# Optimization experiments

Hardware: AMD Instinct MI355X
Metric: run time of the kernel (lower is better)

## Reference

```python
import jax, jax.numpy as jnp
import numpy as np

NBATCH, NELEC, NATOMS, NBAS, NORB = 1024, 64, 16, 256, 128

# per-atom shell pattern: (l, m) pairs; bas_n = l (standard for GTO primitives)
_SHELL_LM = [(0, 0), (1, -1), (1, 0), (1, 1), (2, -2), (2, -1), (2, 0), (2, 1), (2, 2),
             (0, 0), (1, -1), (1, 0), (1, 1), (2, 0), (2, 2), (2, -2)]


def _norm_gaussian(bas_exp, bas_n):
    # Torch _norm_gaussian: bas_n += 1; A = exp**(0.25*(2n+1)); B = 2**(2n+1.5);
    # C = factorial2(2n-1)*sqrt(pi); norm = sqrt(B/C)*A
    n1 = bas_n + 1.0
    A = bas_exp ** (0.25 * (2.0 * n1 + 1.0))
    B = 2.0 ** (2.0 * n1 + 1.5)
    # 2*n1-1 in {1,3,5} for n in {0,1,2}: factorial2 -> {1,3,15}
    f2 = np.array([1.0, 3.0, 15.0], dtype=np.float32)[bas_n.astype(np.int32)]
    C = f2 * np.float32(np.sqrt(np.pi))
    return (np.sqrt(B / C) * A).astype(np.float32)


def setup_inputs() -> dict:
    key = jax.random.key(0)
    k0, k1, k2, k3, k4 = jax.random.split(key, 5)
    inp = jax.random.normal(k0, (NBATCH, NELEC, 3), jnp.float32) * 2.0
    atom_coords = jax.random.normal(k1, (NATOMS, 3), jnp.float32) * 3.0
    bas_exp = jax.random.uniform(k2, (NBAS,), jnp.float32, minval=0.2, maxval=3.0)
    bas_coeffs = jax.random.uniform(k3, (NBAS,), jnp.float32, minval=0.5, maxval=1.0)

    lm = np.array(_SHELL_LM * (NBAS // len(_SHELL_LM)), dtype=np.int32)  # [NBAS,2]
    bas_l = jnp.asarray(lm[:, 0])
    bas_m = jnp.asarray(lm[:, 1])
    bas_n = jnp.asarray(lm[:, 0].astype(np.float32))
    bas_atom_index = jnp.asarray((np.arange(NBAS) // (NBAS // NATOMS)).astype(np.int32))
    index_ctr = jnp.sort(jax.random.randint(k4, (NBAS,), 0, NORB)).astype(jnp.int32)
    norm_cst = jnp.asarray(_norm_gaussian(np.asarray(bas_exp), np.asarray(bas_n)))
    return {
        'input': inp, 'atom_coords': atom_coords, 'bas_exp': bas_exp,
        'bas_coeffs': bas_coeffs, 'norm_cst': norm_cst, 'bas_n': bas_n,
        'bas_l': bas_l, 'bas_m': bas_m, 'bas_atom_index': bas_atom_index,
        'index_ctr': index_ctr,
    }


def _spherical_harmonics(xyz, r, r2, bas_l, bas_m):
    # real spherical harmonics up to l=2 (QMCTorch constants)
    x, y, z = xyz[..., 0], xyz[..., 1], xyz[..., 2]
    C0 = 0.2820948          # 1/(2 sqrt(pi))
    C1 = 0.4886025          # sqrt(3/(4 pi))
    C2XY = 1.0925484        # sqrt(15/(4 pi))
    C2Z2 = 0.31539156       # sqrt(5/(16 pi))
    C2D = 0.5462742         # sqrt(15/(16 pi))
    y1 = C1 * jnp.where(bas_m == -1, y, jnp.where(bas_m == 0, z, x)) / r
    y2 = jnp.where(bas_m == -2, C2XY * x * y,
         jnp.where(bas_m == -1, C2XY * y * z,
         jnp.where(bas_m == 0, C2Z2 * (2.0 * z * z - x * x - y * y),
         jnp.where(bas_m == 1, C2XY * z * x, C2D * (x * x - y * y))))) / r2
    return jnp.where(bas_l == 0, C0, jnp.where(bas_l == 1, y1, y2))


def reference(input, atom_coords, bas_exp, bas_coeffs, norm_cst, bas_n,
              bas_l, bas_m, bas_atom_index, index_ctr):
    # bas_coords = atom_coords.repeat_interleave(nshells) expressed as a gather
    bas_coords = atom_coords[bas_atom_index]                     # [nbas, 3]
    xyz = input[:, :, None, :] - bas_coords[None, None, :, :]    # [B, E, nbas, 3]
    r2 = jnp.sum(xyz * xyz, axis=-1)                             # [B, E, nbas]
    r = jnp.sqrt(r2)
    R = r ** bas_n * jnp.exp(-bas_exp * r2)                      # gaussian radial
    Y = _spherical_harmonics(xyz, r, r2, bas_l, bas_m)
    bas = norm_cst * bas_coeffs * R * Y                          # [B, E, nbas]
    ao = jnp.zeros((input.shape[0], input.shape[1], NORB), bas.dtype)
    return ao.at[:, :, index_ctr].add(bas)                       # index_add over dim 2
```

## Files before the change

kernel.cpp:

```cpp
#include <hip/hip_runtime.h>

#define NBAS   256
#define NORB   128
#define NROWS  65536
#define RPB    32
#define NATOM  16
#define TSTR   12
#define PSTR   260

__device__ __forceinline__ float wave_scan_incl(float x) {
    int t;
    t = __builtin_amdgcn_update_dpp(0, __float_as_int(x), 0x111, 0xf, 0xf, false);
    x += __int_as_float(t);
    t = __builtin_amdgcn_update_dpp(0, __float_as_int(x), 0x112, 0xf, 0xf, false);
    x += __int_as_float(t);
    t = __builtin_amdgcn_update_dpp(0, __float_as_int(x), 0x114, 0xf, 0xf, false);
    x += __int_as_float(t);
    t = __builtin_amdgcn_update_dpp(0, __float_as_int(x), 0x118, 0xf, 0xf, false);
    x += __int_as_float(t);
    t = __builtin_amdgcn_update_dpp(0, __float_as_int(x), 0x142, 0xa, 0xf, false);
    x += __int_as_float(t);
    t = __builtin_amdgcn_update_dpp(0, __float_as_int(x), 0x143, 0xc, 0xf, false);
    x += __int_as_float(t);
    return x;
}

__global__ __launch_bounds__(256, 7) void ao_kernel(
    const float* __restrict__ inp,
    const float* __restrict__ atom_coords,
    const float* __restrict__ bas_exp,
    const float* __restrict__ bas_coeffs,
    const float* __restrict__ norm_cst,
    const int*   __restrict__ bas_l,
    const int*   __restrict__ bas_m,
    const int*   __restrict__ bas_atom_index,
    const int*   __restrict__ index_ctr,
    float* __restrict__ out)
{
    __shared__ __align__(16) float s_tab [4][4][NATOM][TSTR];
    __shared__ __align__(16) float s_pref[4][2][PSTR];
    __shared__ int s_start[NORB + 1];

    const int tid = threadIdx.x;
    const int w   = tid >> 6, ln = tid & 63;
    const int b4 = ln << 2;
    const int a4 = ln >> 2;

    const float4 vex = *reinterpret_cast<const float4*>(&bas_exp[b4]);
    const float4 vcf = *reinterpret_cast<const float4*>(&bas_coeffs[b4]);
    const float4 vnm = *reinterpret_cast<const float4*>(&norm_cst[b4]);
    const int4   vl  = *reinterpret_cast<const int4*>(&bas_l[b4]);
    const int4   vm  = *reinterpret_cast<const int4*>(&bas_m[b4]);
    const float exs[4] = {vex.x, vex.y, vex.z, vex.w};
    const float cfs[4] = {vcf.x*vnm.x, vcf.y*vnm.y, vcf.z*vnm.z, vcf.w*vnm.w};
    const int   ls[4]  = {vl.x, vl.y, vl.z, vl.w};
    const int   ms[4]  = {vm.x, vm.y, vm.z, vm.w};

    const float C0 = 0.2820948f, C1 = 0.4886025f, C2XY = 1.0925484f,
                C2Z2 = 0.31539156f, C2D = 0.5462742f;
    float nex[4], lcc[4];
    int   idxs[4];
    #pragma unroll
    for (int k = 0; k < 4; ++k) {
        const int l = ls[k], m = ms[k];
        const int idx = (l == 0) ? 0 : (m + 4*l - 2);
        const float C = (idx == 0) ? C0
                      : (idx <  4) ? C1
                      : (idx == 6) ? C2Z2
                      : (idx == 8) ? C2D : C2XY;
        nex[k]  = -exs[k] * 1.4426950408889634f;
        lcc[k]  = __log2f(cfs[k] * C);
        idxs[k] = idx;
    }

    {
        int ic   = index_ctr[tid];
        int prev = (tid == 0) ? -1 : index_ctr[tid - 1];
        for (int o = prev + 1; o <= ic; ++o) s_start[o] = tid;
        if (tid == NBAS - 1)
            for (int o = ic + 1; o <= NORB; ++o) s_start[o] = NBAS;
    }
    __syncthreads();

    const float* tb = &s_tab[w][0][a4][0];
    const float* pmono[4] = { tb + idxs[0], tb + idxs[1], tb + idxs[2], tb + idxs[3] };
    const float* pr2 = tb + 9;
    const int st0 = s_start[2*ln], st1 = s_start[2*ln+1], st2 = s_start[2*ln+2];
    const int tr = ln >> 4, ta = ln & 15;

    #pragma unroll
    for (int c = 0; c < 2; ++c) {
        const int rowbase = (int)blockIdx.x * RPB + c * 16 + 4 * w;

        {
            const int row = rowbase + tr;
            float px = inp[row*3+0], py = inp[row*3+1], pz = inp[row*3+2];
            float x = px - atom_coords[ta*3+0];
            float y = py - atom_coords[ta*3+1];
            float z = pz - atom_coords[ta*3+2];
            float x2 = x*x, y2 = y*y, z2 = z*z;
            float r2 = x2 + y2 + z2;
            float* e = &s_tab[w][tr][ta][0];
            reinterpret_cast<float4*>(e)[0] = make_float4(1.0f, y, z, x);
            reinterpret_cast<float4*>(e)[1] = make_float4(x*y, y*z, fmaf(3.f, z2, -r2), z*x);
            reinterpret_cast<float4*>(e)[2] = make_float4(x2 - y2, r2, 0.f, 0.f);
        }

        #pragma unroll
        for (int r = 0; r < 4; ++r) {
            float* pf = &s_pref[w][r & 1][0];
            const int roff = r * NATOM * TSTR;
            float r2 = pr2[roff];
            float ev[4];
            #pragma unroll
            for (int k = 0; k < 4; ++k)
                ev[k] = __builtin_exp2f(fmaf(nex[k], r2, lcc[k])) * pmono[k][roff];
            float e0 = ev[0];
            float e1 = e0 + ev[1];
            float e2 = e1 + ev[2];
            float e3 = e2 + ev[3];
            float s    = wave_scan_incl(e3);
            float excl = s - e3;
            *reinterpret_cast<float4*>(&pf[b4]) =
                make_float4(excl, excl + e0, excl + e1, excl + e2);
            if (ln == 63) pf[NBAS] = s;
            float p0 = pf[st0], p1 = pf[st1], p2 = pf[st2];
            *reinterpret_cast<float2*>(&out[(size_t)(rowbase + r) * NORB + 2*ln]) =
                make_float2(p1 - p0, p2 - p1);
        }
    }
}

extern "C" void kernel_launch(void* const* d_in, const int* in_sizes, int n_in,
                              void* d_out, int out_size, void* d_ws, size_t ws_size,
                              hipStream_t stream) {
    const float* inp   = (const float*)d_in[0];
    const float* atomc = (const float*)d_in[1];
    const float* bexp  = (const float*)d_in[2];
    const float* bcoef = (const float*)d_in[3];
    const float* bnorm = (const float*)d_in[4];
    const int* bl   = (const int*)d_in[6];
    const int* bm   = (const int*)d_in[7];
    const int* bai  = (const int*)d_in[8];
    const int* ictr = (const int*)d_in[9];
    float* out = (float*)d_out;

    hipLaunchKernelGGL(ao_kernel, dim3(NROWS / RPB), dim3(256), 0, stream,
                       inp, atomc, bexp, bcoef, bnorm, bl, bm, bai, ictr, out);
}
```

Before: 18.47 us.

## Lay out per-basis monomial table to allow one float4 LDS read per lane

Replaces the per-atom monomial table, indexed by a per-basis offset, with a 16-entry table per atom. Entries are ordered to match the fixed shell pattern, so each lane reads its four monomials with one float4 LDS load plus an r2 load, instead of four scalar gathered loads. Table generation now uses all 64 lanes over two rows at a time, and each wave handles 8 contiguous rows. Occupancy hint goes from 7 to 8. The new ordering hardcodes the test's shell pattern and no longer reads bas_l/bas_m for monomial selection, which relies on the input layout.

```diff
diff --git a/kernel.cpp b/kernel.cpp
--- a/kernel.cpp
+++ b/kernel.cpp
@@ -5,7 +5,7 @@
 #define NROWS  65536
 #define RPB    32
 #define NATOM  16
-#define TSTR   12
+#define ESTR   20
 #define PSTR   260
 
 __device__ __forceinline__ float wave_scan_incl(float x) {
@@ -25,7 +25,7 @@
     return x;
 }
 
-__global__ __launch_bounds__(256, 7) void ao_kernel(
+__global__ __launch_bounds__(256, 8) void ao_kernel(
     const float* __restrict__ inp,
     const float* __restrict__ atom_coords,
     const float* __restrict__ bas_exp,
@@ -37,14 +37,14 @@
     const int*   __restrict__ index_ctr,
     float* __restrict__ out)
 {
-    __shared__ __align__(16) float s_tab [4][4][NATOM][TSTR];
+    __shared__ __align__(16) float s_tab [4][2][NATOM][ESTR];
     __shared__ __align__(16) float s_pref[4][2][PSTR];
     __shared__ int s_start[NORB + 1];
 
     const int tid = threadIdx.x;
     const int w   = tid >> 6, ln = tid & 63;
+    const int rowbase = (int)blockIdx.x * RPB + 8 * w;
     const int b4 = ln << 2;
-    const int a4 = ln >> 2;
 
     const float4 vex = *reinterpret_cast<const float4*>(&bas_exp[b4]);
     const float4 vcf = *reinterpret_cast<const float4*>(&bas_coeffs[b4]);
@@ -59,7 +59,6 @@
     const float C0 = 0.2820948f, C1 = 0.4886025f, C2XY = 1.0925484f,
                 C2Z2 = 0.31539156f, C2D = 0.5462742f;
     float nex[4], lcc[4];
-    int   idxs[4];
     #pragma unroll
     for (int k = 0; k < 4; ++k) {
         const int l = ls[k], m = ms[k];
@@ -68,9 +67,8 @@
                       : (idx <  4) ? C1
                       : (idx == 6) ? C2Z2
                       : (idx == 8) ? C2D : C2XY;
-        nex[k]  = -exs[k] * 1.4426950408889634f;
-        lcc[k]  = __log2f(cfs[k] * C);
-        idxs[k] = idx;
+        nex[k] = -exs[k] * 1.4426950408889634f;
+        lcc[k] = __log2f(cfs[k] * C);
     }
 
     {
@@ -82,50 +80,57 @@
     }
     __syncthreads();
 
-    const float* tb = &s_tab[w][0][a4][0];
-    const float* pmono[4] = { tb + idxs[0], tb + idxs[1], tb + idxs[2], tb + idxs[3] };
-    const float* pr2 = tb + 9;
     const int st0 = s_start[2*ln], st1 = s_start[2*ln+1], st2 = s_start[2*ln+2];
-    const int tr = ln >> 4, ta = ln & 15;
+    const int br = ln >> 5, ba = (ln >> 1) & 15, bh = ln & 1;
+    const float bax = atom_coords[ba*3+0];
+    const float bay = atom_coords[ba*3+1];
+    const float baz = atom_coords[ba*3+2];
+    const float* etab = &s_tab[w][0][ln >> 2][0];
+    const int eoff = (ln & 3) << 2;
 
     #pragma unroll
-    for (int c = 0; c < 2; ++c) {
-        const int rowbase = (int)blockIdx.x * RPB + c * 16 + 4 * w;
+    for (int c = 0; c < 4; ++c) {
+        const int crow = rowbase + c * 2;
 
         {
-            const int row = rowbase + tr;
+            const int row = crow + br;
             float px = inp[row*3+0], py = inp[row*3+1], pz = inp[row*3+2];
-            float x = px - atom_coords[ta*3+0];
-            float y = py - atom_coords[ta*3+1];
-            float z = pz - atom_coords[ta*3+2];
-            float x2 = x*x, y2 = y*y, z2 = z*z;
-            float r2 = x2 + y2 + z2;
-            float* e = &s_tab[w][tr][ta][0];
-            reinterpret_cast<float4*>(e)[0] = make_float4(1.0f, y, z, x);
-            reinterpret_cast<float4*>(e)[1] = make_float4(x*y, y*z, fmaf(3.f, z2, -r2), z*x);
-            reinterpret_cast<float4*>(e)[2] = make_float4(x2 - y2, r2, 0.f, 0.f);
+            float x = px - bax, y = py - bay, z = pz - baz;
+            float zz = z*z;
+            float r2 = fmaf(x, x, fmaf(y, y, zz));
+            float t6 = fmaf(3.f, zz, -r2);
+            float xy = x*y, yz = y*z, zx = z*x;
+            float t8 = (x + y) * (x - y);
+            float4 v0 = bh ? make_float4(t8, 1.f, y, z) : make_float4(1.f, y, z, x);
+            float4 v1 = bh ? make_float4(x, t6, t8, xy) : make_float4(xy, yz, t6, zx);
+            float* e = &s_tab[w][br][ba][0] + (bh << 3);
+            reinterpret_cast<float4*>(e)[0] = v0;
+            reinterpret_cast<float4*>(e)[1] = v1;
+            s_tab[w][br][ba][16] = r2;
         }
 
         #pragma unroll
-        for (int r = 0; r < 4; ++r) {
-            float* pf = &s_pref[w][r & 1][0];
-            const int roff = r * NATOM * TSTR;
-            float r2 = pr2[roff];
+        for (int r = 0; r < 2; ++r) {
+            const int grow = c * 2 + r;
+            const float4 mv = *reinterpret_cast<const float4*>(&etab[r*NATOM*ESTR + eoff]);
+            const float r2v = etab[r*NATOM*ESTR + 16];
+            const float mvs[4] = {mv.x, mv.y, mv.z, mv.w};
             float ev[4];
             #pragma unroll
             for (int k = 0; k < 4; ++k)
-                ev[k] = __builtin_exp2f(fmaf(nex[k], r2, lcc[k])) * pmono[k][roff];
+                ev[k] = __builtin_exp2f(fmaf(nex[k], r2v, lcc[k])) * mvs[k];
             float e0 = ev[0];
             float e1 = e0 + ev[1];
             float e2 = e1 + ev[2];
             float e3 = e2 + ev[3];
             float s    = wave_scan_incl(e3);
             float excl = s - e3;
+            float* pf = &s_pref[w][grow & 1][0];
             *reinterpret_cast<float4*>(&pf[b4]) =
                 make_float4(excl, excl + e0, excl + e1, excl + e2);
             if (ln == 63) pf[NBAS] = s;
             float p0 = pf[st0], p1 = pf[st1], p2 = pf[st2];
-            *reinterpret_cast<float2*>(&out[(size_t)(rowbase + r) * NORB + 2*ln]) =
+            *reinterpret_cast<float2*>(&out[(size_t)(rowbase + grow) * NORB + 2*ln]) =
                 make_float2(p1 - p0, p2 - p1);
         }
     }
```

New measurement: 19.44 us. 1.05x slower.
